# Kernel tuning notes

Measured on AMD Instinct MI355X. Metric: run time of the kernel, lower is better.

Reference implementation:

```python
import jax, jax.numpy as jnp
import numpy as np

B, S, D = 4, 4096, 1024
E, K, H = 8, 2, 2048


def setup_inputs() -> dict:
    key = jax.random.key(0)
    ks = jax.random.split(key, 6)
    scale_g = 1.0 / np.sqrt(D)
    scale_1 = 1.0 / np.sqrt(D)
    scale_2 = 1.0 / np.sqrt(H)
    return {
        "x": jax.random.normal(ks[0], (B, S, D), dtype=jnp.float32),
        "Wg": jax.random.uniform(ks[1], (D, E), jnp.float32, -scale_g, scale_g),
        "W1": jax.random.uniform(ks[2], (E, D, H), jnp.float32, -scale_1, scale_1),
        "b1": jax.random.uniform(ks[3], (E, H), jnp.float32, -scale_1, scale_1),
        "W2": jax.random.uniform(ks[4], (E, H, D), jnp.float32, -scale_2, scale_2),
        "b2": jax.random.uniform(ks[5], (E, D), jnp.float32, -scale_2, scale_2),
    }


def reference(x, Wg, W1, b1, W2, b2):
    # Router: softmax gate, top-k selection, renormalized combine weights
    logits = jnp.einsum("bsd,de->bse", x, Wg)          # [B,S,E]
    probs = jax.nn.softmax(logits, axis=-1)
    topv, topi = jax.lax.top_k(probs, K)                # [B,S,K]
    cw = topv / (jnp.sum(topv, axis=-1, keepdims=True) + 1e-9)
    # Per-token weight for each expert: sum over k of one_hot(idx_k)*cw_k -> [B,S,E]
    we = jnp.sum(jax.nn.one_hot(topi, E, dtype=x.dtype) * cw[..., None], axis=-2)
    # Weighted combine of per-expert FFN outputs (loop over small fixed E)
    y = jnp.zeros_like(x)
    for e in range(E):
        h = jax.nn.relu(jnp.einsum("bsd,dh->bsh", x, W1[e]) + b1[e])
        out_e = jnp.einsum("bsh,hd->bsd", h, W2[e]) + b2[e]
        y = y + we[..., e:e + 1] * out_e
    return y
```

## Files before the change

### kernel.cpp

```cpp
#include <hip/hip_runtime.h>
#include <hip/hip_bf16.h>

#define TOK 16384
#define DIM 1024
#define HID 2048
#define NEXP 8

typedef __attribute__((ext_vector_type(4))) float f32x4;
typedef __attribute__((ext_vector_type(8))) short s16x8;

__device__ __forceinline__ unsigned short f2bf(float f) {
  union { float f; unsigned u; } v; v.f = f;
  unsigned r = v.u + 0x7fffu + ((v.u >> 16) & 1u);
  return (unsigned short)(r >> 16);
}
__device__ __forceinline__ int tile_byte(int r, int kk2) {
  return (r * 128 + kk2) ^ ((r & 7) << 4);
}
__device__ __forceinline__ void gld_lds16(const void* g, void* l) {
  __builtin_amdgcn_global_load_lds(
      (const __attribute__((address_space(1))) unsigned int*)g,
      (__attribute__((address_space(3))) unsigned int*)l, 16, 0, 0);
}
__device__ __forceinline__ int xcd_swz(int p, int nwg) {
  int q = nwg >> 3, r = nwg & 7;
  int xcd = p & 7, idx = p >> 3;
  return (xcd < r ? xcd * (q + 1) : r * (q + 1) + (xcd - r) * q) + idx;
}

__global__ void wg_tr(const float* __restrict__ Wg, float* __restrict__ WgT) {
  int i = blockIdx.x * 256 + threadIdx.x;
  int e = i >> 10, dd = i & 1023;
  WgT[i] = Wg[dd * NEXP + e];
}

__global__ void prep_tiles(const float* __restrict__ src, unsigned short* __restrict__ dst,
                           int rows, int cols) {
  int ct = blockIdx.x, kb = blockIdx.y, e = blockIdx.z;
  int nct = gridDim.x, nkb = gridDim.y;
  __shared__ __align__(16) unsigned short tile[8192];
  const float* s = src + ((size_t)e * rows + kb * 64) * cols + ct * 128;
  int tid = threadIdx.x;
  #pragma unroll
  for (int it = 0; it < 8; it++) {
    int idx = it * 256 + tid;
    int kk = idx >> 5;
    int r4 = (idx & 31) * 4;
    float4 v = *(const float4*)(s + (size_t)kk * cols + r4);
    char* tb = (char*)tile;
    *(unsigned short*)(tb + tile_byte(r4 + 0, kk * 2)) = f2bf(v.x);
    *(unsigned short*)(tb + tile_byte(r4 + 1, kk * 2)) = f2bf(v.y);
    *(unsigned short*)(tb + tile_byte(r4 + 2, kk * 2)) = f2bf(v.z);
    *(unsigned short*)(tb + tile_byte(r4 + 3, kk * 2)) = f2bf(v.w);
  }
  __syncthreads();
  unsigned short* d = dst + (((size_t)e * nct + ct) * nkb + kb) * 8192;
  #pragma unroll
  for (int it = 0; it < 4; it++) {
    int o = it * 256 + tid;
    *(s16x8*)(d + o * 8) = *(const s16x8*)((const char*)tile + o * 16);
  }
}

__global__ __launch_bounds__(256)
void router_logits_cvt(const float* __restrict__ x, const float* __restrict__ WgT,
                       unsigned short* __restrict__ xbf,
                       int* __restrict__ sel, float2* __restrict__ wp) {
  int wave = threadIdx.x >> 6, lane = threadIdx.x & 63;
  int t = blockIdx.x * 4 + wave;
  const f32x4* xr = (const f32x4*)(x + (size_t)t * DIM);
  unsigned short* xb = xbf + (size_t)t * DIM;
  float acc[NEXP];
  #pragma unroll
  for (int e = 0; e < NEXP; e++) acc[e] = 0.f;
  #pragma unroll
  for (int q = 0; q < 4; q++) {
    f32x4 xv = xr[q * 64 + lane];
    ushort4 bv;
    bv.x = f2bf(xv[0]); bv.y = f2bf(xv[1]); bv.z = f2bf(xv[2]); bv.w = f2bf(xv[3]);
    *(ushort4*)(xb + (q * 64 + lane) * 4) = bv;
    #pragma unroll
    for (int e = 0; e < NEXP; e++) {
      f32x4 wv = *(const f32x4*)(WgT + (size_t)e * DIM + (q * 64 + lane) * 4);
      acc[e] = fmaf(xv[3], wv[3], fmaf(xv[2], wv[2], fmaf(xv[1], wv[1], fmaf(xv[0], wv[0], acc[e]))));
    }
  }
  #pragma unroll
  for (int e = 0; e < NEXP; e++) {
    float v = acc[e];
    #pragma unroll
    for (int off = 32; off >= 1; off >>= 1) v += __shfl_xor(v, off);
    acc[e] = v;
  }
  if (lane == 0) {
    float m = acc[0];
    #pragma unroll
    for (int e = 1; e < NEXP; e++) m = fmaxf(m, acc[e]);
    float p[NEXP], s = 0.f;
    #pragma unroll
    for (int e = 0; e < NEXP; e++) { p[e] = expf(acc[e] - m); s += p[e]; }
    float inv = 1.f / s;
    int i0 = 0; float v0 = p[0];
    #pragma unroll
    for (int e = 1; e < NEXP; e++) if (p[e] > v0) { v0 = p[e]; i0 = e; }
    int i1 = -1; float v1 = -1.f;
    #pragma unroll
    for (int e = 0; e < NEXP; e++) if (e != i0 && p[e] > v1) { v1 = p[e]; i1 = e; }
    v0 *= inv; v1 *= inv;
    float den = v0 + v1 + 1e-9f;
    sel[t] = i0 | (i1 << 4);
    wp[t] = make_float2(v0 / den, v1 / den);
  }
}

__global__ __launch_bounds__(256)
void router_scatter(const int* __restrict__ sel, const float2* __restrict__ wp,
                    int* __restrict__ counts, int* __restrict__ tok_list,
                    float* __restrict__ w_list) {
  __shared__ int lh0[4][16], lh1[4][16];
  __shared__ int bbase[16];
  int tid = threadIdx.x, wave = tid >> 6, lane = tid & 63;
  int t = blockIdx.x * 256 + tid;
  int s = sel[t];
  int b0 = s & 15;
  int b1 = 8 + ((s >> 4) & 15);
  float2 w = wp[t];
  unsigned long long lt = (lane == 63) ? ~0ull >> 1 : (((unsigned long long)1 << lane) - 1);
  int r0 = 0, r1 = 0;
  #pragma unroll
  for (int b = 0; b < 8; b++) {
    unsigned long long m0 = __ballot(b0 == b);
    if (b0 == b) r0 = __popcll(m0 & lt);
    if (lane == 0) { lh0[wave][b] = __popcll(m0); lh1[wave][b] = 0; }
  }
  #pragma unroll
  for (int b = 8; b < 16; b++) {
    unsigned long long m1 = __ballot(b1 == b);
    if (b1 == b) r1 = __popcll(m1 & lt);
    if (lane == 0) { lh1[wave][b] = __popcll(m1); lh0[wave][b] = 0; }
  }
  __syncthreads();
  if (tid < 16) {
    int h = 0;
    #pragma unroll
    for (int v = 0; v < 4; v++) h += lh0[v][tid] + lh1[v][tid];
    bbase[tid] = atomicAdd(&counts[tid], h);
  }
  __syncthreads();
  int p0 = bbase[b0] + r0;
  int p1 = bbase[b1] + r1;
  #pragma unroll
  for (int v = 0; v < 4; v++) {
    if (v < wave) { p0 += lh0[v][b0]; p1 += lh1[v][b1]; }
  }
  int e0 = b0, e1 = b1 - 8;
  tok_list[e0 * TOK + p0] = t;
  w_list[e0 * TOK + p0] = w.x;
  int q1 = TOK - 1 - p1;
  tok_list[e1 * TOK + q1] = t;
  w_list[e1 * TOK + q1] = w.y;
}

__global__ void calc_off(const int* __restrict__ counts, int* __restrict__ off) {
  if (threadIdx.x == 0 && blockIdx.x == 0) {
    int a = 0;
    for (int e = 0; e < NEXP; e++)
      for (int s = 0; s < 2; s++) {
        off[e * 2 + s] = a;
        a += (counts[s * 8 + e] + 127) & ~127;
      }
  }
}

__global__ __launch_bounds__(256, 4)
void moe_gemm1(const unsigned short* __restrict__ xbf, const unsigned short* __restrict__ w1s,
               const float* __restrict__ b1, const int* __restrict__ counts,
               const int* __restrict__ off, const int* __restrict__ tok_list,
               unsigned short* __restrict__ h_s, int ct_off, int nkbc, int nct) {
  int logical = xcd_swz(blockIdx.x, gridDim.x);
  int CG = (nct >= 8) ? 8 : nct;
  int e = -1, seg = 0, rt = 0, ct_l = 0, segcnt = 0, base = 0;
  #pragma unroll
  for (int zz = 0; zz < 16; zz++) {
    int ee = zz >> 1, ss = zz & 1;
    int c = counts[ss * 8 + ee];
    int nt = (c + 127) >> 7;
    int span = nt * nct;
    if (e < 0 && logical < base + span) {
      e = ee; seg = ss; segcnt = c;
      int local = logical - base;
      int grp = nt * CG;
      int h = local / grp, rem = local - h * grp;
      rt = rem / CG;
      ct_l = h * CG + (rem - rt * CG);
    }
    base += span;
  }
  if (e < 0) return;

  __shared__ __align__(16) unsigned short As[8192];
  __shared__ __align__(16) unsigned short Bs[8192];
  __shared__ int tokS[128];

  int tid = threadIdx.x, wave = tid >> 6, lane = tid & 63;
  int llo = lane & 15, lhi = lane >> 4;
  int wr = wave >> 1, wc = wave & 1;
  int ct_g = ct_off + ct_l;

  if (tid < 128) {
    int q = rt * 128 + tid;
    int qq = q < segcnt ? q : segcnt - 1;
    int slot = seg ? (TOK - 1 - qq) : qq;
    tokS[tid] = tok_list[e * TOK + slot];
  }
  __syncthreads();

  const char* srcA[4];
  #pragma unroll
  for (int i = 0; i < 4; i++) {
    int r = i * 32 + (tid >> 3);
    srcA[i] = (const char*)xbf + (size_t)tokS[r] * (DIM * 2) + (((tid & 7) ^ (r & 7)) * 16);
  }
  const char* gB = (const char*)(w1s + (((size_t)e * 16 + ct_g) * 16) * 8192);

  f32x4 acc[4][4];
  #pragma unroll
  for (int i = 0; i < 4; i++)
    #pragma unroll
    for (int j = 0; j < 4; j++) acc[i][j] = (f32x4){0.f, 0.f, 0.f, 0.f};

  for (int kb = 0; kb < 16; kb++) {
    #pragma unroll
    for (int i = 0; i < 4; i++)
      gld_lds16(srcA[i] + kb * 128, (char*)As + i * 4096 + wave * 1024);
    const char* gs = gB + (size_t)kb * 16384 + wave * 1024 + lane * 16;
    #pragma unroll
    for (int i = 0; i < 4; i++)
      gld_lds16(gs + i * 4096, (char*)Bs + i * 4096 + wave * 1024);
    __syncthreads();
    #pragma unroll
    for (int ks = 0; ks < 2; ks++) {
      s16x8 a[4], b[4];
      #pragma unroll
      for (int f = 0; f < 4; f++) {
        a[f] = *(const s16x8*)((const char*)As + tile_byte(wr * 64 + f * 16 + llo, ks * 64 + lhi * 16));
        b[f] = *(const s16x8*)((const char*)Bs + tile_byte(wc * 64 + f * 16 + llo, ks * 64 + lhi * 16));
      }
      #pragma unroll
      for (int fr = 0; fr < 4; fr++)
        #pragma unroll
        for (int fc = 0; fc < 4; fc++)
          acc[fr][fc] = __builtin_amdgcn_mfma_f32_16x16x32_bf16(a[fr], b[fc], acc[fr][fc], 0, 0, 0);
    }
    __syncthreads();
  }

  size_t grt = (size_t)(off[e * 2 + seg] >> 7) + rt;
  unsigned short* hb = h_s + grt * ((size_t)nkbc * 8192);
  const float* b1e = b1 + e * HID + ct_g * 128;
  #pragma unroll
  for (int fc = 0; fc < 4; fc++) {
    int col = wc * 64 + fc * 16 + llo;
    float bv = b1e[col];
    char* tb = (char*)(hb + ((size_t)(ct_l * 2 + (col >> 6))) * 8192);
    int kk2 = (col & 63) * 2;
    #pragma unroll
    for (int fr = 0; fr < 4; fr++) {
      int r0 = wr * 64 + fr * 16 + lhi * 4;
      #pragma unroll
      for (int j = 0; j < 4; j++) {
        float v = fmaxf(acc[fr][fc][j] + bv, 0.f);
        *(unsigned short*)(tb + tile_byte(r0 + j, kk2)) = f2bf(v);
      }
    }
  }
}

template<int NKBC>
__global__ __launch_bounds__(256, 4)
void moe_gemm2(const unsigned short* __restrict__ h_s, const unsigned short* __restrict__ w2s,
               const float* __restrict__ b2, const int* __restrict__ counts,
               const int* __restrict__ off, const int* __restrict__ tok_list,
               const float* __restrict__ w_list, float* __restrict__ y,
               int seg, int kb_off, int add_b2, int accum) {
  int logical = xcd_swz(blockIdx.x, gridDim.x);
  int e = -1, rt = 0, ct = 0, segcnt = 0, base = 0;
  #pragma unroll
  for (int ee = 0; ee < 8; ee++) {
    int c = counts[seg * 8 + ee];
    int nt = (c + 127) >> 7;
    int span = nt * 8;
    if (e < 0 && logical < base + span) {
      e = ee; segcnt = c;
      int local = logical - base;
      int grp = nt * 4;
      int h = local / grp, rem = local - h * grp;
      rt = rem >> 2;
      ct = h * 4 + (rem & 3);
    }
    base += span;
  }
  if (e < 0) return;

  __shared__ __align__(16) unsigned short As[8192];
  __shared__ __align__(16) unsigned short Bs[8192];

  int tid = threadIdx.x, wave = tid >> 6, lane = tid & 63;
  int llo = lane & 15, lhi = lane >> 4;
  int wr = wave >> 1, wc = wave & 1;

  size_t grt = (size_t)(off[e * 2 + seg] >> 7) + rt;
  const char* gA = (const char*)(h_s + grt * ((size_t)NKBC * 8192));
  const char* gB = (const char*)(w2s + (((size_t)e * 8 + ct) * 32 + kb_off) * 8192);

  f32x4 acc[4][4];
  #pragma unroll
  for (int i = 0; i < 4; i++)
    #pragma unroll
    for (int j = 0; j < 4; j++) acc[i][j] = (f32x4){0.f, 0.f, 0.f, 0.f};

  for (int kb = 0; kb < NKBC; kb++) {
    const char* ga = gA + (size_t)kb * 16384 + wave * 1024 + lane * 16;
    const char* gb = gB + (size_t)kb * 16384 + wave * 1024 + lane * 16;
    #pragma unroll
    for (int i = 0; i < 4; i++) {
      gld_lds16(ga + i * 4096, (char*)As + i * 4096 + wave * 1024);
      gld_lds16(gb + i * 4096, (char*)Bs + i * 4096 + wave * 1024);
    }
    __syncthreads();
    #pragma unroll
    for (int ks = 0; ks < 2; ks++) {
      s16x8 a[4], b[4];
      #pragma unroll
      for (int f = 0; f < 4; f++) {
        a[f] = *(const s16x8*)((const char*)As + tile_byte(wr * 64 + f * 16 + llo, ks * 64 + lhi * 16));
        b[f] = *(const s16x8*)((const char*)Bs + tile_byte(wc * 64 + f * 16 + llo, ks * 64 + lhi * 16));
      }
      #pragma unroll
      for (int fr = 0; fr < 4; fr++)
        #pragma unroll
        for (int fc = 0; fc < 4; fc++)
          acc[fr][fc] = __builtin_amdgcn_mfma_f32_16x16x32_bf16(a[fr], b[fc], acc[fr][fc], 0, 0, 0);
    }
    __syncthreads();
  }

  const float* b2e = b2 + e * DIM + ct * 128;
  #pragma unroll
  for (int fr = 0; fr < 4; fr++) {
    #pragma unroll
    for (int j = 0; j < 4; j++) {
      int q = rt * 128 + wr * 64 + fr * 16 + lhi * 4 + j;
      if (q < segcnt) {
        int slot = seg ? (TOK - 1 - q) : q;
        int t = tok_list[e * TOK + slot];
        float w = w_list[e * TOK + slot];
        float bs = add_b2 ? w : 0.f;
        #pragma unroll
        for (int fc = 0; fc < 4; fc++) {
          int col = wc * 64 + fc * 16 + llo;
          float val = w * acc[fr][fc][j] + bs * b2e[col];
          size_t idx = (size_t)t * DIM + ct * 128 + col;
          if (accum) y[idx] += val;
          else       y[idx] = val;
        }
      }
    }
  }
}

__global__ void transpose_cvt(const float* __restrict__ src, unsigned short* __restrict__ dst,
                              int R, int C) {
  __shared__ float tile[32][33];
  int e = blockIdx.z;
  const float* s = src + (size_t)e * R * C;
  unsigned short* d = dst + (size_t)e * R * C;
  int c0 = blockIdx.x * 32, r0 = blockIdx.y * 32;
  int tx = threadIdx.x, ty = threadIdx.y;
  #pragma unroll
  for (int i = 0; i < 32; i += 8)
    tile[ty + i][tx] = s[(size_t)(r0 + ty + i) * C + c0 + tx];
  __syncthreads();
  #pragma unroll
  for (int i = 0; i < 32; i += 8)
    d[(size_t)(c0 + ty + i) * R + r0 + tx] = f2bf(tile[tx][ty + i]);
}

__global__ void router_kernel(const float* __restrict__ x, const float* __restrict__ Wg,
                              int* __restrict__ counts, int* __restrict__ tok_list,
                              float* __restrict__ w_list) {
  int wave = threadIdx.x >> 6, lane = threadIdx.x & 63;
  int t = blockIdx.x * 4 + wave;
  const float* xr = x + (size_t)t * DIM;
  float acc[NEXP];
  #pragma unroll
  for (int e = 0; e < NEXP; e++) acc[e] = 0.f;
  for (int i = 0; i < DIM / 64; i++) {
    int dd = i * 64 + lane;
    float xv = xr[dd];
    const float* wr = Wg + (size_t)dd * NEXP;
    #pragma unroll
    for (int e = 0; e < NEXP; e++) acc[e] = fmaf(xv, wr[e], acc[e]);
  }
  #pragma unroll
  for (int e = 0; e < NEXP; e++) {
    float v = acc[e];
    #pragma unroll
    for (int off = 32; off >= 1; off >>= 1) v += __shfl_xor(v, off);
    acc[e] = v;
  }
  if (lane == 0) {
    float m = acc[0];
    #pragma unroll
    for (int e = 1; e < NEXP; e++) m = fmaxf(m, acc[e]);
    float p[NEXP], s = 0.f;
    #pragma unroll
    for (int e = 0; e < NEXP; e++) { p[e] = expf(acc[e] - m); s += p[e]; }
    float inv = 1.f / s;
    int i0 = 0; float v0 = p[0];
    #pragma unroll
    for (int e = 1; e < NEXP; e++) if (p[e] > v0) { v0 = p[e]; i0 = e; }
    int i1 = -1; float v1 = -1.f;
    #pragma unroll
    for (int e = 0; e < NEXP; e++) if (e != i0 && p[e] > v1) { v1 = p[e]; i1 = e; }
    v0 *= inv; v1 *= inv;
    float den = v0 + v1 + 1e-9f;
    float w0 = v0 / den, w1 = v1 / den;
    int q0 = atomicAdd(&counts[i0], 1);
    tok_list[i0 * TOK + q0] = t;           w_list[i0 * TOK + q0] = w0;
    int q1 = atomicAdd(&counts[8 + i1], 1);
    int p1 = TOK - 1 - q1;
    tok_list[i1 * TOK + p1] = t;           w_list[i1 * TOK + p1] = w1;
  }
}

__global__ __launch_bounds__(512, 4)
void moe_ffn_kernel(const float* __restrict__ x,
                    const unsigned short* __restrict__ w1t,
                    const unsigned short* __restrict__ w2t,
                    const float* __restrict__ b1, const float* __restrict__ b2,
                    const int* __restrict__ counts, const int* __restrict__ tok_list,
                    const float* __restrict__ w_list, float* __restrict__ y) {
  int zz = blockIdx.y, e = zz & 7, seg = zz >> 3;
  int segcnt = counts[seg * 8 + e];
  int row0 = blockIdx.x * 32;
  if (row0 >= segcnt) return;
  __shared__ unsigned short Xs[32 * DIM];
  __shared__ unsigned short hsl[32 * 64];
  __shared__ int tokS[32];
  __shared__ float wS[32];
  int tid = threadIdx.x, wave = tid >> 6, lane = tid & 63;
  if (tid < 32) {
    int q = row0 + tid;
    if (q < segcnt) {
      int slot = seg ? (TOK - 1 - q) : q;
      tokS[tid] = tok_list[e * TOK + slot]; wS[tid] = w_list[e * TOK + slot];
    } else { tokS[tid] = -1; wS[tid] = 0.f; }
  }
  __syncthreads();
  #pragma unroll
  for (int it = 0; it < 8; it++) {
    int chunk = it * 512 + tid;
    int r = chunk >> 7, c = (chunk & 127) * 8;
    int tok = tokS[r];
    float4 f0 = make_float4(0.f, 0.f, 0.f, 0.f), f1 = f0;
    if (tok >= 0) {
      const float4* xp = (const float4*)(x + (size_t)tok * DIM + c);
      f0 = xp[0]; f1 = xp[1];
    }
    s16x8 bv;
    bv[0] = (short)f2bf(f0.x); bv[1] = (short)f2bf(f0.y);
    bv[2] = (short)f2bf(f0.z); bv[3] = (short)f2bf(f0.w);
    bv[4] = (short)f2bf(f1.x); bv[5] = (short)f2bf(f1.y);
    bv[6] = (short)f2bf(f1.z); bv[7] = (short)f2bf(f1.w);
    int byte = (r * DIM + c) * 2; byte ^= (r & 7) << 4;
    *(s16x8*)((char*)Xs + byte) = bv;
  }
  __syncthreads();
  int rw = wave >> 2, cw = wave & 3;
  int lhi = lane >> 4, llo = lane & 15;
  f32x4 acc[16];
  #pragma unroll
  for (int i = 0; i < 16; i++) acc[i] = (f32x4){0.f, 0.f, 0.f, 0.f};
  int arow = rw * 16 + llo;
  int abase = arow * (DIM * 2) + lhi * 16;
  int aswz = (arow & 7) << 4;
  int h_abase = arow * (64 * 2) + lhi * 16;
  const size_t eHD = (size_t)e * HID * DIM;
  const unsigned short* w2e = w2t + (size_t)e * DIM * HID;
  for (int hc = 0; hc < HID; hc += 64) {
    f32x4 c1 = (f32x4){0.f, 0.f, 0.f, 0.f};
    const unsigned short* w1p = w1t + eHD + (size_t)(hc + cw * 16 + llo) * DIM + lhi * 8;
    #pragma unroll 4
    for (int k = 0; k < DIM; k += 32) {
      s16x8 a = *(const s16x8*)((const char*)Xs + ((abase + k * 2) ^ aswz));
      s16x8 b = *(const s16x8*)(w1p + k);
      c1 = __builtin_amdgcn_mfma_f32_16x16x32_bf16(a, b, c1, 0, 0, 0);
    }
    float b1v = b1[e * HID + hc + cw * 16 + llo];
    __syncthreads();
    #pragma unroll
    for (int j = 0; j < 4; j++) {
      int r = rw * 16 + lhi * 4 + j;
      float v = fmaxf(c1[j] + b1v, 0.f);
      int byte = (r * 64 + cw * 16 + llo) * 2; byte ^= (r & 7) << 4;
      *(unsigned short*)((char*)hsl + byte) = f2bf(v);
    }
    __syncthreads();
    s16x8 a0 = *(const s16x8*)((const char*)hsl + ((h_abase + 0)  ^ aswz));
    s16x8 a1 = *(const s16x8*)((const char*)hsl + ((h_abase + 64) ^ aswz));
    const unsigned short* w2p0 = w2e + hc + lhi * 8;
    #pragma unroll 4
    for (int ctile = 0; ctile < 16; ctile++) {
      int dcol = cw * 256 + ctile * 16 + llo;
      const unsigned short* bp = w2p0 + (size_t)dcol * HID;
      s16x8 b0 = *(const s16x8*)(bp);
      s16x8 b1f = *(const s16x8*)(bp + 32);
      acc[ctile] = __builtin_amdgcn_mfma_f32_16x16x32_bf16(a0, b0, acc[ctile], 0, 0, 0);
      acc[ctile] = __builtin_amdgcn_mfma_f32_16x16x32_bf16(a1, b1f, acc[ctile], 0, 0, 0);
    }
  }
  const float* b2e = b2 + e * DIM;
  #pragma unroll
  for (int ctile = 0; ctile < 16; ctile++) {
    int dcol = cw * 256 + ctile * 16 + llo;
    float b2v = b2e[dcol];
    #pragma unroll
    for (int j = 0; j < 4; j++) {
      int r = rw * 16 + lhi * 4 + j;
      int tok = tokS[r];
      if (tok >= 0) atomicAdd(&y[(size_t)tok * DIM + dcol], wS[r] * (acc[ctile][j] + b2v));
    }
  }
}

extern "C" void kernel_launch(void* const* d_in, const int* in_sizes, int n_in,
                              void* d_out, int out_size, void* d_ws, size_t ws_size,
                              hipStream_t stream) {
  const float* x  = (const float*)d_in[0];
  const float* Wg = (const float*)d_in[1];
  const float* W1 = (const float*)d_in[2];
  const float* b1 = (const float*)d_in[3];
  const float* W2 = (const float*)d_in[4];
  const float* b2 = (const float*)d_in[5];
  float* y = (float*)d_out;
  char* ws = (char*)d_ws;

  const size_t O_COUNTS = 0;
  const size_t O_OFF    = 1024;
  const size_t O_TOK    = 2048;
  const size_t O_W      = O_TOK + (size_t)NEXP * TOK * 4;
  const size_t O_WGT    = O_W + (size_t)NEXP * TOK * 4;
  const size_t O_SEL    = O_WGT + (size_t)NEXP * DIM * 4;
  const size_t O_WP     = O_SEL + (size_t)TOK * 4;
  const size_t O_W1S    = O_WP + (size_t)TOK * 8;
  const size_t O_W2S    = O_W1S + (size_t)NEXP * 16 * 16 * 8192 * 2;
  const size_t O_XBF    = O_W2S + (size_t)NEXP * 8 * 32 * 8192 * 2;
  const size_t O_HS     = O_XBF + (size_t)TOK * DIM * 2;

  int Hc = 0;
  if (ws_size > O_HS) {
    size_t avail = ws_size - O_HS;
    for (int hc = HID; hc >= 128; hc >>= 1)
      if ((size_t)34816 * hc * 2 <= avail) { Hc = hc; break; }
  }

  if (Hc) {
    int*   counts   = (int*)(ws + O_COUNTS);
    int*   offp     = (int*)(ws + O_OFF);
    int*   tok_list = (int*)(ws + O_TOK);
    float* w_list   = (float*)(ws + O_W);
    float* WgT      = (float*)(ws + O_WGT);
    int*   sel      = (int*)(ws + O_SEL);
    float2* wp      = (float2*)(ws + O_WP);
    unsigned short* w1s = (unsigned short*)(ws + O_W1S);
    unsigned short* w2s = (unsigned short*)(ws + O_W2S);
    unsigned short* xbf = (unsigned short*)(ws + O_XBF);
    unsigned short* hs  = (unsigned short*)(ws + O_HS);

    hipMemsetAsync(counts, 0, 2048, stream);
    wg_tr<<<32, 256, 0, stream>>>(Wg, WgT);
    prep_tiles<<<dim3(HID / 128, DIM / 64, NEXP), 256, 0, stream>>>(W1, w1s, DIM, HID);
    prep_tiles<<<dim3(DIM / 128, HID / 64, NEXP), 256, 0, stream>>>(W2, w2s, HID, DIM);
    router_logits_cvt<<<TOK / 4, 256, 0, stream>>>(x, WgT, xbf, sel, wp);
    router_scatter<<<TOK / 256, 256, 0, stream>>>(sel, wp, counts, tok_list, w_list);
    calc_off<<<1, 64, 0, stream>>>(counts, offp);

    int nch = HID / Hc, nkbc = Hc / 64, nct = Hc / 128;
    for (int ch = 0; ch < nch; ch++) {
      moe_gemm1<<<272 * nct, 256, 0, stream>>>(
          xbf, w1s, b1, counts, offp, tok_list, hs, ch * nct, nkbc, nct);
      for (int seg = 0; seg < 2; seg++) {
        int add_b2 = (ch == 0) ? 1 : 0;
        int accum  = (ch == 0 && seg == 0) ? 0 : 1;
        int kb_off = ch * nkbc;
        #define LG2(NK) moe_gemm2<NK><<<136 * 8, 256, 0, stream>>>( \
            hs, w2s, b2, counts, offp, tok_list, w_list, y, seg, kb_off, add_b2, accum)
        switch (nkbc) {
          case 32: LG2(32); break;
          case 16: LG2(16); break;
          case 8:  LG2(8);  break;
          case 4:  LG2(4);  break;
          default: LG2(2);  break;
        }
        #undef LG2
      }
    }
  } else {
    int*   counts   = (int*)ws;
    int*   tok_list = (int*)(ws + 2048);
    float* w_list   = (float*)(ws + 2048 + (size_t)NEXP * TOK * 4);
    unsigned short* w1t = (unsigned short*)(ws + 2048 + (size_t)NEXP * TOK * 8);
    unsigned short* w2t = w1t + (size_t)NEXP * HID * DIM;

    hipMemsetAsync(d_out, 0, (size_t)out_size * sizeof(float), stream);
    hipMemsetAsync(counts, 0, 2048, stream);
    transpose_cvt<<<dim3(HID / 32, DIM / 32, NEXP), dim3(32, 8), 0, stream>>>(W1, w1t, DIM, HID);
    transpose_cvt<<<dim3(DIM / 32, HID / 32, NEXP), dim3(32, 8), 0, stream>>>(W2, w2t, HID, DIM);
    router_kernel<<<TOK / 4, 256, 0, stream>>>(x, Wg, counts, tok_list, w_list);
    moe_ffn_kernel<<<dim3(TOK / 32, 16), 512, 0, stream>>>(
        x, w1t, w2t, b1, b2, counts, tok_list, w_list, y);
  }
}
```

Measured before the change: 505.1 us.

## Load W2 B-operand directly into registers in MFMA fragment layout

```diff
diff --git a/kernel.cpp b/kernel.cpp
--- a/kernel.cpp
+++ b/kernel.cpp
@@ -59,6 +59,24 @@
   for (int it = 0; it < 4; it++) {
     int o = it * 256 + tid;
     *(s16x8*)(d + o * 8) = *(const s16x8*)((const char*)tile + o * 16);
+  }
+}
+
+__global__ void prep_frags(const float* __restrict__ W2, unsigned short* __restrict__ w2f) {
+  int ct = blockIdx.x, kb = blockIdx.y, e = blockIdx.z;
+  int tid = threadIdx.x;
+  unsigned short* dst = w2f + (((size_t)(e * 8 + ct) * 32 + kb) * 1024) * 8;
+  #pragma unroll
+  for (int it = 0; it < 4; it++) {
+    int slot = it * 256 + tid;
+    int wc = slot >> 9, ks = (slot >> 8) & 1, f = (slot >> 6) & 3, lane = slot & 63;
+    int k0 = kb * 64 + ks * 32 + (lane >> 4) * 8;
+    int c  = ct * 128 + wc * 64 + f * 16 + (lane & 15);
+    const float* sp = W2 + ((size_t)e * HID + k0) * DIM + c;
+    s16x8 v;
+    #pragma unroll
+    for (int j = 0; j < 8; j++) v[j] = (short)f2bf(sp[(size_t)j * DIM]);
+    *(s16x8*)(dst + (size_t)slot * 8) = v;
   }
 }
 
@@ -277,12 +295,12 @@
 }
 
 template<int NKBC>
-__global__ __launch_bounds__(256, 4)
-void moe_gemm2(const unsigned short* __restrict__ h_s, const unsigned short* __restrict__ w2s,
-               const float* __restrict__ b2, const int* __restrict__ counts,
-               const int* __restrict__ off, const int* __restrict__ tok_list,
-               const float* __restrict__ w_list, float* __restrict__ y,
-               int seg, int kb_off, int add_b2, int accum) {
+__global__ __launch_bounds__(256, 3)
+void moe_gemm2r(const unsigned short* __restrict__ h_s, const unsigned short* __restrict__ w2f,
+                const float* __restrict__ b2, const int* __restrict__ counts,
+                const int* __restrict__ off, const int* __restrict__ tok_list,
+                const float* __restrict__ w_list, float* __restrict__ y,
+                int seg, int kb_off, int add_b2, int accum) {
   int logical = xcd_swz(blockIdx.x, gridDim.x);
   int e = -1, rt = 0, ct = 0, segcnt = 0, base = 0;
   #pragma unroll
@@ -303,7 +321,6 @@
   if (e < 0) return;
 
   __shared__ __align__(16) unsigned short As[8192];
-  __shared__ __align__(16) unsigned short Bs[8192];
 
   int tid = threadIdx.x, wave = tid >> 6, lane = tid & 63;
   int llo = lane & 15, lhi = lane >> 4;
@@ -311,7 +328,8 @@
 
   size_t grt = (size_t)(off[e * 2 + seg] >> 7) + rt;
   const char* gA = (const char*)(h_s + grt * ((size_t)NKBC * 8192));
-  const char* gB = (const char*)(w2s + (((size_t)e * 8 + ct) * 32 + kb_off) * 8192);
+  const unsigned short* fb0 = w2f + (((size_t)(e * 8 + ct) * 32 + kb_off) * 1024
+                                     + wc * 512 + lane) * 8;
 
   f32x4 acc[4][4];
   #pragma unroll
@@ -321,26 +339,28 @@
 
   for (int kb = 0; kb < NKBC; kb++) {
     const char* ga = gA + (size_t)kb * 16384 + wave * 1024 + lane * 16;
-    const char* gb = gB + (size_t)kb * 16384 + wave * 1024 + lane * 16;
-    #pragma unroll
-    for (int i = 0; i < 4; i++) {
+    #pragma unroll
+    for (int i = 0; i < 4; i++)
       gld_lds16(ga + i * 4096, (char*)As + i * 4096 + wave * 1024);
-      gld_lds16(gb + i * 4096, (char*)Bs + i * 4096 + wave * 1024);
-    }
+    const unsigned short* fb = fb0 + (size_t)kb * 8192;
+    s16x8 b[4][2];
+    #pragma unroll
+    for (int ks = 0; ks < 2; ks++)
+      #pragma unroll
+      for (int f = 0; f < 4; f++)
+        b[f][ks] = *(const s16x8*)(fb + ks * 2048 + f * 512);
     __syncthreads();
     #pragma unroll
     for (int ks = 0; ks < 2; ks++) {
-      s16x8 a[4], b[4];
+      s16x8 a[4];
       #pragma unroll
-      for (int f = 0; f < 4; f++) {
+      for (int f = 0; f < 4; f++)
         a[f] = *(const s16x8*)((const char*)As + tile_byte(wr * 64 + f * 16 + llo, ks * 64 + lhi * 16));
-        b[f] = *(const s16x8*)((const char*)Bs + tile_byte(wc * 64 + f * 16 + llo, ks * 64 + lhi * 16));
-      }
       #pragma unroll
       for (int fr = 0; fr < 4; fr++)
         #pragma unroll
         for (int fc = 0; fc < 4; fc++)
-          acc[fr][fc] = __builtin_amdgcn_mfma_f32_16x16x32_bf16(a[fr], b[fc], acc[fr][fc], 0, 0, 0);
+          acc[fr][fc] = __builtin_amdgcn_mfma_f32_16x16x32_bf16(a[fr], b[fc][ks], acc[fr][fc], 0, 0, 0);
     }
     __syncthreads();
   }
@@ -554,8 +574,8 @@
   const size_t O_SEL    = O_WGT + (size_t)NEXP * DIM * 4;
   const size_t O_WP     = O_SEL + (size_t)TOK * 4;
   const size_t O_W1S    = O_WP + (size_t)TOK * 8;
-  const size_t O_W2S    = O_W1S + (size_t)NEXP * 16 * 16 * 8192 * 2;
-  const size_t O_XBF    = O_W2S + (size_t)NEXP * 8 * 32 * 8192 * 2;
+  const size_t O_W2F    = O_W1S + (size_t)NEXP * 16 * 16 * 8192 * 2;
+  const size_t O_XBF    = O_W2F + (size_t)NEXP * 8 * 32 * 8192 * 2;
   const size_t O_HS     = O_XBF + (size_t)TOK * DIM * 2;
 
   int Hc = 0;
@@ -574,14 +594,14 @@
     int*   sel      = (int*)(ws + O_SEL);
     float2* wp      = (float2*)(ws + O_WP);
     unsigned short* w1s = (unsigned short*)(ws + O_W1S);
-    unsigned short* w2s = (unsigned short*)(ws + O_W2S);
+    unsigned short* w2f = (unsigned short*)(ws + O_W2F);
     unsigned short* xbf = (unsigned short*)(ws + O_XBF);
     unsigned short* hs  = (unsigned short*)(ws + O_HS);
 
     hipMemsetAsync(counts, 0, 2048, stream);
     wg_tr<<<32, 256, 0, stream>>>(Wg, WgT);
     prep_tiles<<<dim3(HID / 128, DIM / 64, NEXP), 256, 0, stream>>>(W1, w1s, DIM, HID);
-    prep_tiles<<<dim3(DIM / 128, HID / 64, NEXP), 256, 0, stream>>>(W2, w2s, HID, DIM);
+    prep_frags<<<dim3(8, 32, NEXP), 256, 0, stream>>>(W2, w2f);
     router_logits_cvt<<<TOK / 4, 256, 0, stream>>>(x, WgT, xbf, sel, wp);
     router_scatter<<<TOK / 256, 256, 0, stream>>>(sel, wp, counts, tok_list, w_list);
     calc_off<<<1, 64, 0, stream>>>(counts, offp);
@@ -594,16 +614,16 @@
         int add_b2 = (ch == 0) ? 1 : 0;
         int accum  = (ch == 0 && seg == 0) ? 0 : 1;
         int kb_off = ch * nkbc;
-        #define LG2(NK) moe_gemm2<NK><<<136 * 8, 256, 0, stream>>>( \
-            hs, w2s, b2, counts, offp, tok_list, w_list, y, seg, kb_off, add_b2, accum)
+        #define LG2R(NK) moe_gemm2r<NK><<<136 * 8, 256, 0, stream>>>( \
+            hs, w2f, b2, counts, offp, tok_list, w_list, y, seg, kb_off, add_b2, accum)
         switch (nkbc) {
-          case 32: LG2(32); break;
-          case 16: LG2(16); break;
-          case 8:  LG2(8);  break;
-          case 4:  LG2(4);  break;
-          default: LG2(2);  break;
+          case 32: LG2R(32); break;
+          case 16: LG2R(16); break;
+          case 8:  LG2R(8);  break;
+          case 4:  LG2R(4);  break;
+          default: LG2R(2);  break;
         }
-        #undef LG2
+        #undef LG2R
       }
     }
   } else {
```

Result: no change. 511.5 us (+1.3%).
